# Optimization experiments

Hardware: AMD Instinct MI355X
Metric: run time of the kernel (lower is better)

The kernel has to match this reference:

```python
import jax, jax.numpy as jnp
import numpy as np

INPUT_DIM = 1024
QUERY_DIM = 1024
KEY_DIM = 1024
VALUE_DIM = 1024


def setup_inputs() -> dict:
    key = jax.random.key(0)
    ks = jax.random.split(key, 7)
    B, N = 4, 2048
    s_in = 1.0 / np.sqrt(INPUT_DIM)
    return {
        "x": jax.random.normal(ks[0], (B, N, INPUT_DIM), dtype=jnp.float32),
        "Wq": jax.random.uniform(ks[1], (INPUT_DIM, QUERY_DIM), jnp.float32, -s_in, s_in),
        "bq": jax.random.uniform(ks[2], (QUERY_DIM,), jnp.float32, -s_in, s_in),
        "Wk": jax.random.uniform(ks[3], (INPUT_DIM, KEY_DIM), jnp.float32, -s_in, s_in),
        "bk": jax.random.uniform(ks[4], (KEY_DIM,), jnp.float32, -s_in, s_in),
        "Wv": jax.random.uniform(ks[5], (INPUT_DIM, VALUE_DIM), jnp.float32, -s_in, s_in),
        "bv": jax.random.uniform(ks[6], (VALUE_DIM,), jnp.float32, -s_in, s_in),
    }


def reference(x, Wq, bq, Wk, bk, Wv, bv):
    # projections: (B, N, D)
    q = jnp.einsum("bnd,de->bne", x, Wq) + bq
    k = jnp.einsum("bnd,de->bne", x, Wk) + bk
    v = jnp.einsum("bnd,de->bne", x, Wv) + bv
    scale = 1.0 / jnp.sqrt(jnp.float32(QUERY_DIM))
    scores = jnp.einsum("bqe,bke->bqk", q, k) * scale  # (B, N, N)
    attn = jax.nn.softmax(scores, axis=2)
    return jnp.einsum("bqk,bkv->bqv", attn, v)
```

## Files before the change

kernel.cpp:

```cpp
#include <hip/hip_runtime.h>
#include <hip/hip_bf16.h>

typedef __bf16 bf16x8 __attribute__((ext_vector_type(8)));
typedef float  f32x4  __attribute__((ext_vector_type(4)));

__device__ __forceinline__ void gload16(const __bf16* g, __bf16* l) {
  __builtin_amdgcn_global_load_lds(
      (const __attribute__((address_space(1))) void*)g,
      (__attribute__((address_space(3))) void*)l, 16, 0, 0);
}

__device__ __forceinline__ void stage_tile(const __bf16* __restrict__ g, int ld,
                                           __bf16* l, int wid, int lane) {
#pragma unroll
  for (int p = 0; p < 4; ++p) {
    int c    = p * 256 + wid * 64 + lane;
    int row  = c >> 3;
    int slog = (c & 7) ^ (row & 7);
    gload16(g + (long)row * ld + slog * 8,
            l + (p * 256 + wid * 64) * 8);
  }
}

__device__ __forceinline__ void stage256(const __bf16* __restrict__ g, int ld,
                                         __bf16* l, int wid, int lane) {
#pragma unroll
  for (int p = 0; p < 4; ++p) {
    int c    = p * 512 + wid * 64 + lane;
    int row  = c >> 3;
    int slog = (c & 7) ^ (row & 7);
    gload16(g + (long)row * ld + slog * 8, l + (p * 512 + wid * 64) * 8);
  }
}

__device__ __forceinline__ int lds_off(int r, int s) {
  return r * 128 + ((s * 16) ^ ((r & 7) << 4));
}

template <int OUTBF16, int BIASMODE, int DOSCALE>
__global__ __launch_bounds__(512) void gemm256(
    const __bf16* __restrict__ A, const __bf16* __restrict__ Bt,
    const float* __restrict__ bias, const float* __restrict__ bias2,
    void* __restrict__ Cv, int lda, int ldb, int ldc, int K,
    long sA, long sB, long sC, float scale) {
  __shared__ __align__(16) __bf16 lds[2][2][256 * 64];

  const int tid = threadIdx.x, wid = tid >> 6, lane = tid & 63;
  const int wr = wid >> 2, wc = wid & 3;
  const int rl = lane & 15;

  const int gx = gridDim.x, gy = gridDim.y;
  const int nwg = gx * gy * (int)gridDim.z;
  int flat = ((int)blockIdx.z * gy + (int)blockIdx.y) * gx + (int)blockIdx.x;
  flat = (flat & 7) * (nwg >> 3) + (flat >> 3);
  const int bx = flat % gx;
  const int by = (flat / gx) % gy;
  const int bz = flat / (gx * gy);

  const long brow = (long)by * 256;
  const long bcol = (long)bx * 256;
  const __bf16* ga = A + bz * sA + brow * lda;
  const __bf16* gb = Bt + bz * sB + bcol * ldb;
  const int nk = K >> 6;

  f32x4 acc[8][4];
#pragma unroll
  for (int m = 0; m < 8; ++m)
#pragma unroll
    for (int n = 0; n < 4; ++n) acc[m][n] = (f32x4){0.f, 0.f, 0.f, 0.f};

  stage256(ga, lda, &lds[0][0][0], wid, lane);
  stage256(gb, ldb, &lds[0][1][0], wid, lane);
  __syncthreads();

  for (int kt = 0; kt < nk; ++kt) {
    const int cur = kt & 1;
    if (kt + 1 < nk) {
      stage256(ga + (kt + 1) * 64, lda, &lds[cur ^ 1][0][0], wid, lane);
      stage256(gb + (kt + 1) * 64, ldb, &lds[cur ^ 1][1][0], wid, lane);
    }
    const char* Ab = (const char*)&lds[cur][0][0];
    const char* Bb = (const char*)&lds[cur][1][0];
#pragma unroll
    for (int ks = 0; ks < 2; ++ks) {
      const int s = ks * 4 + (lane >> 4);
      bf16x8 af[8], bf[4];
#pragma unroll
      for (int m = 0; m < 8; ++m)
        af[m] = *(const bf16x8*)(Ab + lds_off(wr * 128 + m * 16 + rl, s));
#pragma unroll
      for (int n = 0; n < 4; ++n)
        bf[n] = *(const bf16x8*)(Bb + lds_off(wc * 64 + n * 16 + rl, s));
#pragma unroll
      for (int m = 0; m < 8; ++m)
#pragma unroll
        for (int n = 0; n < 4; ++n)
          acc[m][n] = __builtin_amdgcn_mfma_f32_16x16x32_bf16(af[m], bf[n],
                                                              acc[m][n], 0, 0, 0);
    }
    __syncthreads();
  }

  const long cb = (long)bz * sC;
#pragma unroll
  for (int m = 0; m < 8; ++m) {
    const int row = (int)brow + wr * 128 + m * 16 + ((lane >> 4) << 2);
#pragma unroll
    for (int n = 0; n < 4; ++n) {
      const int col = (int)bcol + wc * 64 + n * 16 + rl;
#pragma unroll
      for (int r = 0; r < 4; ++r) {
        float v = acc[m][n][r];
        if (DOSCALE) v *= scale;
        if (BIASMODE == 1) v += (col < 1024) ? bias[col] : bias2[col - 1024];
        if (BIASMODE == 2) v += bias[row + r];
        if (OUTBF16)
          ((__bf16*)Cv)[cb + (long)(row + r) * ldc + col] = (__bf16)v;
        else
          ((float*)Cv)[cb + (long)(row + r) * ldc + col] = v;
      }
    }
  }
}

template <int OUTBF16, int BIASMODE, int DOSCALE>
__global__ __launch_bounds__(256) void gemm8(
    const __bf16* __restrict__ A, const __bf16* __restrict__ Bt,
    const float* __restrict__ bias, const float* __restrict__ bias2,
    void* __restrict__ Cv, int lda, int ldb, int ldc, int K,
    long sA, long sB, long sC, float scale) {
  __shared__ __align__(16) __bf16 lds[2][2][128 * 64];

  const int tid = threadIdx.x, wid = tid >> 6, lane = tid & 63;
  const int wr = wid >> 1, wc = wid & 1;

  const int gx = gridDim.x, gy = gridDim.y;
  const int nwg = gx * gy * (int)gridDim.z;
  int flat = ((int)blockIdx.z * gy + (int)blockIdx.y) * gx + (int)blockIdx.x;
  flat = (flat & 7) * (nwg >> 3) + (flat >> 3);
  const int bx = flat % gx;
  const int by = (flat / gx) % gy;
  const int bz = flat / (gx * gy);

  const long brow = (long)by * 128;
  const long bcol = (long)bx * 128;
  const __bf16* ga = A + bz * sA + brow * lda;
  const __bf16* gb = Bt + bz * sB + bcol * ldb;
  const int nk = K >> 6;

  f32x4 acc[4][4];
#pragma unroll
  for (int m = 0; m < 4; ++m)
#pragma unroll
    for (int n = 0; n < 4; ++n) acc[m][n] = (f32x4){0.f, 0.f, 0.f, 0.f};

  stage_tile(ga, lda, &lds[0][0][0], wid, lane);
  stage_tile(gb, ldb, &lds[0][1][0], wid, lane);
  __syncthreads();

  for (int kt = 0; kt < nk; ++kt) {
    const int cur = kt & 1;
    if (kt + 1 < nk) {
      stage_tile(ga + (kt + 1) * 64, lda, &lds[cur ^ 1][0][0], wid, lane);
      stage_tile(gb + (kt + 1) * 64, ldb, &lds[cur ^ 1][1][0], wid, lane);
    }
    const char* Ab = (const char*)&lds[cur][0][0];
    const char* Bb = (const char*)&lds[cur][1][0];
#pragma unroll
    for (int ks = 0; ks < 2; ++ks) {
      bf16x8 af[4], bfr[4];
      const int s = ks * 4 + (lane >> 4);
#pragma unroll
      for (int m = 0; m < 4; ++m)
        af[m] = *(const bf16x8*)(Ab + lds_off(wr * 64 + m * 16 + (lane & 15), s));
#pragma unroll
      for (int n = 0; n < 4; ++n)
        bfr[n] = *(const bf16x8*)(Bb + lds_off(wc * 64 + n * 16 + (lane & 15), s));
#pragma unroll
      for (int m = 0; m < 4; ++m)
#pragma unroll
        for (int n = 0; n < 4; ++n)
          acc[m][n] = __builtin_amdgcn_mfma_f32_16x16x32_bf16(
              af[m], bfr[n], acc[m][n], 0, 0, 0);
    }
    __syncthreads();
  }

  const long cb = (long)bz * sC;
#pragma unroll
  for (int m = 0; m < 4; ++m) {
    const int row = (int)brow + wr * 64 + m * 16 + ((lane >> 4) << 2);
#pragma unroll
    for (int n = 0; n < 4; ++n) {
      const int col = (int)bcol + wc * 64 + n * 16 + (lane & 15);
#pragma unroll
      for (int r = 0; r < 4; ++r) {
        float v = acc[m][n][r];
        if (DOSCALE) v *= scale;
        if (BIASMODE == 1) v += (col < 1024) ? bias[col] : bias2[col - 1024];
        if (BIASMODE == 2) v += bias[row + r];
        if (OUTBF16)
          ((__bf16*)Cv)[cb + (long)(row + r) * ldc + col] = (__bf16)v;
        else
          ((float*)Cv)[cb + (long)(row + r) * ldc + col] = v;
      }
    }
  }
}

__global__ __launch_bounds__(256) void convert_x(const float* __restrict__ x,
                                                 __bf16* __restrict__ o) {
  const long i = ((long)blockIdx.x * 256 + threadIdx.x) * 16;
#pragma unroll
  for (int h = 0; h < 2; ++h) {
    float4 a = *(const float4*)(x + i + h * 8);
    float4 b = *(const float4*)(x + i + h * 8 + 4);
    bf16x8 v;
    v[0] = (__bf16)a.x; v[1] = (__bf16)a.y; v[2] = (__bf16)a.z; v[3] = (__bf16)a.w;
    v[4] = (__bf16)b.x; v[5] = (__bf16)b.y; v[6] = (__bf16)b.z; v[7] = (__bf16)b.w;
    *(bf16x8*)(o + i + h * 8) = v;
  }
}

__global__ __launch_bounds__(256) void transpose_w(
    const float* __restrict__ W0, const float* __restrict__ W1,
    const float* __restrict__ W2, __bf16* __restrict__ T0,
    __bf16* __restrict__ T1, __bf16* __restrict__ T2) {
  const float* W = blockIdx.z == 0 ? W0 : (blockIdx.z == 1 ? W1 : W2);
  __bf16* T      = blockIdx.z == 0 ? T0 : (blockIdx.z == 1 ? T1 : T2);
  __shared__ float t[64][65];
  const int e0 = blockIdx.x * 64, d0 = blockIdx.y * 64;
  const int tr = threadIdx.x >> 2, tc = (threadIdx.x & 3) * 16;
  const float* src = W + (long)(d0 + tr) * 1024 + e0 + tc;
#pragma unroll
  for (int i = 0; i < 4; ++i) {
    float4 v = *(const float4*)(src + i * 4);
    t[tr][tc + i * 4 + 0] = v.x;
    t[tr][tc + i * 4 + 1] = v.y;
    t[tr][tc + i * 4 + 2] = v.z;
    t[tr][tc + i * 4 + 3] = v.w;
  }
  __syncthreads();
  __bf16* dst = T + (long)(e0 + tr) * 1024 + d0 + tc;
  bf16x8 v0, v1;
#pragma unroll
  for (int i = 0; i < 8; ++i) v0[i] = (__bf16)t[tc + i][tr];
#pragma unroll
  for (int i = 0; i < 8; ++i) v1[i] = (__bf16)t[tc + 8 + i][tr];
  *(bf16x8*)dst = v0;
  *(bf16x8*)(dst + 8) = v1;
}

__global__ __launch_bounds__(256) void softmax_rows(__bf16* __restrict__ P) {
  __bf16* p = P + (long)blockIdx.x * 2048;
  const int t = threadIdx.x, wid = t >> 6, lane = t & 63;
  bf16x8 v = *(bf16x8*)(p + t * 8);
  float f[8];
  float mx = -1e30f;
#pragma unroll
  for (int i = 0; i < 8; ++i) { f[i] = (float)v[i]; mx = fmaxf(mx, f[i]); }
#pragma unroll
  for (int o = 32; o > 0; o >>= 1) mx = fmaxf(mx, __shfl_xor(mx, o));
  __shared__ float redm[4], reds[4];
  if (lane == 0) redm[wid] = mx;
  __syncthreads();
  mx = fmaxf(fmaxf(redm[0], redm[1]), fmaxf(redm[2], redm[3]));
  float s = 0.f;
#pragma unroll
  for (int i = 0; i < 8; ++i) { f[i] = __expf(f[i] - mx); s += f[i]; }
#pragma unroll
  for (int o = 32; o > 0; o >>= 1) s += __shfl_xor(s, o);
  if (lane == 0) reds[wid] = s;
  __syncthreads();
  s = reds[0] + reds[1] + reds[2] + reds[3];
  const float inv = 1.0f / s;
#pragma unroll
  for (int i = 0; i < 8; ++i) v[i] = (__bf16)(f[i] * inv);
  *(bf16x8*)(p + t * 8) = v;
}

extern "C" void kernel_launch(void* const* d_in, const int* in_sizes, int n_in,
                              void* d_out, int out_size, void* d_ws,
                              size_t ws_size, hipStream_t stream) {
  const float* x  = (const float*)d_in[0];
  const float* Wq = (const float*)d_in[1];
  const float* bq = (const float*)d_in[2];
  const float* Wk = (const float*)d_in[3];
  const float* bk = (const float*)d_in[4];
  const float* Wv = (const float*)d_in[5];
  const float* bv = (const float*)d_in[6];
  float* out = (float*)d_out;

  char* ws = (char*)d_ws;
  __bf16* xb   = (__bf16*)(ws);
  __bf16* wqkt = (__bf16*)(ws + (16l << 20));
  __bf16* wvt  = (__bf16*)(ws + (20l << 20));
  __bf16* qk   = (__bf16*)(ws + (22l << 20));
  __bf16* vt   = (__bf16*)(ws + (54l << 20));
  __bf16* S    = (__bf16*)(ws + (70l << 20));

  convert_x<<<2048, 256, 0, stream>>>(x, xb);
  transpose_w<<<dim3(16, 16, 3), 256, 0, stream>>>(
      Wq, Wk, Wv, wqkt, wqkt + 1024l * 1024, wvt);

  gemm256<1, 1, 0><<<dim3(8, 32, 1), 512, 0, stream>>>(
      xb, wqkt, bq, bk, qk, 1024, 1024, 2048, 1024, 0, 0, 0, 1.f);
  gemm8<1, 2, 0><<<dim3(64, 8, 1), 256, 0, stream>>>(
      wvt, xb, bv, nullptr, vt, 1024, 1024, 8192, 1024, 0, 0, 0, 1.f);

  gemm256<1, 0, 1><<<dim3(8, 8, 4), 512, 0, stream>>>(
      qk, qk + 1024, nullptr, nullptr, S, 2048, 2048, 2048, 1024,
      2048l * 2048, 2048l * 2048, 2048l * 2048, 0.03125f);

  softmax_rows<<<8192, 256, 0, stream>>>(S);

  gemm8<0, 0, 0><<<dim3(8, 16, 4), 256, 0, stream>>>(
      S, vt, nullptr, nullptr, out, 2048, 8192, 1024, 2048,
      2048l * 2048, 2048, 2048l * 1024, 1.f);
}
```

Measured before the change: 158.9 us.

## Replace 256x256 GEMM with eight-phase split-half LDS pipeline

The 256x256-tile bf16 GEMM used for the QK projection and the scores product is rewritten as an eight-phase schedule. The A and B tiles are split into 128-row halves, and each half is refilled by global-to-LDS loads interleaved between MFMA quadrants. Manual s_barrier, vmcnt waits and s_setprio bracket the MFMA clusters, so loads overlap compute at finer grain than the old whole-tile double buffer with one __syncthreads per k-step. This adds many barriers and relies on the hand-counted waitcnt values being correct.

```diff
diff --git a/kernel.cpp b/kernel.cpp
--- a/kernel.cpp
+++ b/kernel.cpp
@@ -10,6 +10,17 @@
       (__attribute__((address_space(3))) void*)l, 16, 0, 0);
 }
 
+__device__ __forceinline__ void stage_half(const __bf16* __restrict__ g, int ld,
+                                           __bf16* l, int wid, int lane) {
+#pragma unroll
+  for (int p = 0; p < 2; ++p) {
+    int c    = p * 512 + wid * 64 + lane;
+    int row  = c >> 3;
+    int slog = (c & 7) ^ (row & 7);
+    gload16(g + (long)row * ld + slog * 8, l + c * 8);
+  }
+}
+
 __device__ __forceinline__ void stage_tile(const __bf16* __restrict__ g, int ld,
                                            __bf16* l, int wid, int lane) {
 #pragma unroll
@@ -17,19 +28,7 @@
     int c    = p * 256 + wid * 64 + lane;
     int row  = c >> 3;
     int slog = (c & 7) ^ (row & 7);
-    gload16(g + (long)row * ld + slog * 8,
-            l + (p * 256 + wid * 64) * 8);
-  }
-}
-
-__device__ __forceinline__ void stage256(const __bf16* __restrict__ g, int ld,
-                                         __bf16* l, int wid, int lane) {
-#pragma unroll
-  for (int p = 0; p < 4; ++p) {
-    int c    = p * 512 + wid * 64 + lane;
-    int row  = c >> 3;
-    int slog = (c & 7) ^ (row & 7);
-    gload16(g + (long)row * ld + slog * 8, l + (p * 512 + wid * 64) * 8);
+    gload16(g + (long)row * ld + slog * 8, l + c * 8);
   }
 }
 
@@ -37,17 +36,20 @@
   return r * 128 + ((s * 16) ^ ((r & 7) << 4));
 }
 
+#define BAR() asm volatile("s_barrier" ::: "memory")
+
 template <int OUTBF16, int BIASMODE, int DOSCALE>
-__global__ __launch_bounds__(512) void gemm256(
+__global__ __launch_bounds__(512) void gemm8ph(
     const __bf16* __restrict__ A, const __bf16* __restrict__ Bt,
     const float* __restrict__ bias, const float* __restrict__ bias2,
     void* __restrict__ Cv, int lda, int ldb, int ldc, int K,
     long sA, long sB, long sC, float scale) {
-  __shared__ __align__(16) __bf16 lds[2][2][256 * 64];
+  __shared__ __align__(16) __bf16 LA[2][2][128 * 64];
+  __shared__ __align__(16) __bf16 LB[2][2][128 * 64];
 
   const int tid = threadIdx.x, wid = tid >> 6, lane = tid & 63;
   const int wr = wid >> 2, wc = wid & 3;
-  const int rl = lane & 15;
+  const int rl = lane & 15, q = lane >> 4;
 
   const int gx = gridDim.x, gy = gridDim.y;
   const int nwg = gx * gy * (int)gridDim.z;
@@ -61,66 +63,128 @@
   const long bcol = (long)bx * 256;
   const __bf16* ga = A + bz * sA + brow * lda;
   const __bf16* gb = Bt + bz * sB + bcol * ldb;
-  const int nk = K >> 6;
-
-  f32x4 acc[8][4];
-#pragma unroll
-  for (int m = 0; m < 8; ++m)
-#pragma unroll
-    for (int n = 0; n < 4; ++n) acc[m][n] = (f32x4){0.f, 0.f, 0.f, 0.f};
-
-  stage256(ga, lda, &lds[0][0][0], wid, lane);
-  stage256(gb, ldb, &lds[0][1][0], wid, lane);
-  __syncthreads();
-
-  for (int kt = 0; kt < nk; ++kt) {
-    const int cur = kt & 1;
-    if (kt + 1 < nk) {
-      stage256(ga + (kt + 1) * 64, lda, &lds[cur ^ 1][0][0], wid, lane);
-      stage256(gb + (kt + 1) * 64, ldb, &lds[cur ^ 1][1][0], wid, lane);
-    }
-    const char* Ab = (const char*)&lds[cur][0][0];
-    const char* Bb = (const char*)&lds[cur][1][0];
-#pragma unroll
-    for (int ks = 0; ks < 2; ++ks) {
-      const int s = ks * 4 + (lane >> 4);
-      bf16x8 af[8], bf[4];
-#pragma unroll
-      for (int m = 0; m < 8; ++m)
-        af[m] = *(const bf16x8*)(Ab + lds_off(wr * 128 + m * 16 + rl, s));
-#pragma unroll
-      for (int n = 0; n < 4; ++n)
-        bf[n] = *(const bf16x8*)(Bb + lds_off(wc * 64 + n * 16 + rl, s));
-#pragma unroll
-      for (int m = 0; m < 8; ++m)
-#pragma unroll
-        for (int n = 0; n < 4; ++n)
-          acc[m][n] = __builtin_amdgcn_mfma_f32_16x16x32_bf16(af[m], bf[n],
-                                                              acc[m][n], 0, 0, 0);
-    }
-    __syncthreads();
+  const int NI = K >> 7;
+
+  f32x4 acc[2][2][4][2];
+#pragma unroll
+  for (int a = 0; a < 2; ++a)
+#pragma unroll
+    for (int b = 0; b < 2; ++b)
+#pragma unroll
+      for (int c = 0; c < 4; ++c)
+#pragma unroll
+        for (int d = 0; d < 2; ++d) acc[a][b][c][d] = (f32x4){0.f, 0.f, 0.f, 0.f};
+
+  stage_half(ga, lda, LA[0][0], wid, lane);
+  stage_half(ga + 128l * lda, lda, LA[0][1], wid, lane);
+  stage_half(gb, ldb, LB[0][0], wid, lane);
+  stage_half(gb + 128l * ldb, ldb, LB[0][1], wid, lane);
+  stage_half(ga + 64, lda, LA[1][0], wid, lane);
+  stage_half(gb + 64, ldb, LB[1][0], wid, lane);
+  asm volatile("s_waitcnt vmcnt(4)" ::: "memory");
+  BAR();
+
+  bf16x8 af[4][2], bf0[2][2], bf1[2][2];
+
+#define LOAD_AF(BASE)                                                       \
+  _Pragma("unroll") for (int i_ = 0; i_ < 4; ++i_)                          \
+      _Pragma("unroll") for (int k_ = 0; k_ < 2; ++k_)                      \
+          af[i_][k_] = *(const bf16x8*)((const char*)(BASE) +               \
+                       lds_off(wr * 64 + i_ * 16 + rl, k_ * 4 + q));
+
+#define LOAD_BF(DST, BASE)                                                  \
+  _Pragma("unroll") for (int n_ = 0; n_ < 2; ++n_)                          \
+      _Pragma("unroll") for (int k_ = 0; k_ < 2; ++k_)                      \
+          DST[n_][k_] = *(const bf16x8*)((const char*)(BASE) +              \
+                        lds_off(wc * 32 + n_ * 16 + rl, k_ * 4 + q));
+
+#define MFMA_Q(MH, NH, BF)                                                  \
+  __builtin_amdgcn_s_setprio(1);                                            \
+  _Pragma("unroll") for (int i_ = 0; i_ < 4; ++i_)                          \
+      _Pragma("unroll") for (int n_ = 0; n_ < 2; ++n_)                      \
+          _Pragma("unroll") for (int k_ = 0; k_ < 2; ++k_)                  \
+              acc[MH][NH][i_][n_] = __builtin_amdgcn_mfma_f32_16x16x32_bf16(\
+                  af[i_][k_], BF[n_][k_], acc[MH][NH][i_][n_], 0, 0, 0);    \
+  __builtin_amdgcn_s_setprio(0);
+
+  for (int it = 0; it < NI; ++it) {
+    const bool full = (it + 1 < NI);
+    const long uo = (long)(2 * it + 1) * 64;
+    const long t2 = (long)(2 * it + 2) * 64;
+    const long u2 = (long)(2 * it + 3) * 64;
+
+    LOAD_AF(LA[0][0]);
+    LOAD_BF(bf0, LB[0][0]);
+    stage_half(ga + 128l * lda + uo, lda, LA[1][1], wid, lane);
+    stage_half(gb + 128l * ldb + uo, ldb, LB[1][1], wid, lane);
+    BAR(); MFMA_Q(0, 0, bf0); BAR();
+
+    LOAD_BF(bf1, LB[0][1]);
+    BAR(); MFMA_Q(0, 1, bf1); BAR();
+
+    LOAD_AF(LA[0][1]);
+    if (full) stage_half(ga + t2, lda, LA[0][0], wid, lane);
+    BAR(); MFMA_Q(1, 0, bf0); BAR();
+
+    if (full) {
+      stage_half(gb + t2, ldb, LB[0][0], wid, lane);
+      asm volatile("s_waitcnt vmcnt(4)" ::: "memory");
+    } else {
+      asm volatile("s_waitcnt vmcnt(0)" ::: "memory");
+    }
+    BAR(); MFMA_Q(1, 1, bf1); BAR();
+
+    LOAD_AF(LA[1][0]);
+    LOAD_BF(bf0, LB[1][0]);
+    if (full) {
+      stage_half(ga + 128l * lda + t2, lda, LA[0][1], wid, lane);
+      stage_half(gb + 128l * ldb + t2, ldb, LB[0][1], wid, lane);
+    }
+    BAR(); MFMA_Q(0, 0, bf0); BAR();
+
+    LOAD_BF(bf1, LB[1][1]);
+    BAR(); MFMA_Q(0, 1, bf1); BAR();
+
+    LOAD_AF(LA[1][1]);
+    if (full) stage_half(ga + u2, lda, LA[1][0], wid, lane);
+    BAR(); MFMA_Q(1, 0, bf0); BAR();
+
+    if (full) {
+      stage_half(gb + u2, ldb, LB[1][0], wid, lane);
+      asm volatile("s_waitcnt vmcnt(4)" ::: "memory");
+    }
+    BAR(); MFMA_Q(1, 1, bf1); BAR();
   }
 
   const long cb = (long)bz * sC;
 #pragma unroll
-  for (int m = 0; m < 8; ++m) {
-    const int row = (int)brow + wr * 128 + m * 16 + ((lane >> 4) << 2);
-#pragma unroll
-    for (int n = 0; n < 4; ++n) {
-      const int col = (int)bcol + wc * 64 + n * 16 + rl;
-#pragma unroll
-      for (int r = 0; r < 4; ++r) {
-        float v = acc[m][n][r];
-        if (DOSCALE) v *= scale;
-        if (BIASMODE == 1) v += (col < 1024) ? bias[col] : bias2[col - 1024];
-        if (BIASMODE == 2) v += bias[row + r];
-        if (OUTBF16)
-          ((__bf16*)Cv)[cb + (long)(row + r) * ldc + col] = (__bf16)v;
-        else
-          ((float*)Cv)[cb + (long)(row + r) * ldc + col] = v;
+  for (int mh = 0; mh < 2; ++mh) {
+#pragma unroll
+    for (int nh = 0; nh < 2; ++nh) {
+#pragma unroll
+      for (int i = 0; i < 4; ++i) {
+        const int row = (int)brow + mh * 128 + wr * 64 + i * 16 + q * 4;
+#pragma unroll
+        for (int n = 0; n < 2; ++n) {
+          const int col = (int)bcol + nh * 128 + wc * 32 + n * 16 + rl;
+#pragma unroll
+          for (int r = 0; r < 4; ++r) {
+            float v = acc[mh][nh][i][n][r];
+            if (DOSCALE) v *= scale;
+            if (BIASMODE == 1) v += (col < 1024) ? bias[col] : bias2[col - 1024];
+            if (BIASMODE == 2) v += bias[row + r];
+            if (OUTBF16)
+              ((__bf16*)Cv)[cb + (long)(row + r) * ldc + col] = (__bf16)v;
+            else
+              ((float*)Cv)[cb + (long)(row + r) * ldc + col] = v;
+          }
+        }
       }
     }
   }
+#undef LOAD_AF
+#undef LOAD_BF
+#undef MFMA_Q
 }
 
 template <int OUTBF16, int BIASMODE, int DOSCALE>
@@ -303,12 +367,12 @@
   transpose_w<<<dim3(16, 16, 3), 256, 0, stream>>>(
       Wq, Wk, Wv, wqkt, wqkt + 1024l * 1024, wvt);
 
-  gemm256<1, 1, 0><<<dim3(8, 32, 1), 512, 0, stream>>>(
+  gemm8ph<1, 1, 0><<<dim3(8, 32, 1), 512, 0, stream>>>(
       xb, wqkt, bq, bk, qk, 1024, 1024, 2048, 1024, 0, 0, 0, 1.f);
   gemm8<1, 2, 0><<<dim3(64, 8, 1), 256, 0, stream>>>(
       wvt, xb, bv, nullptr, vt, 1024, 1024, 8192, 1024, 0, 0, 0, 1.f);
 
-  gemm256<1, 0, 1><<<dim3(8, 8, 4), 512, 0, stream>>>(
+  gemm8ph<1, 0, 1><<<dim3(8, 8, 4), 512, 0, stream>>>(
       qk, qk + 1024, nullptr, nullptr, S, 2048, 2048, 2048, 1024,
       2048l * 2048, 2048l * 2048, 2048l * 2048, 0.03125f);
 
```

New measurement: 167.7 us. 5.6% more time.
